# Kernel tuning notes

Measured on AMD Instinct MI355X. Metric: run time of the kernel, lower is better.

The kernel has to match this reference:

```python
import jax, jax.numpy as jnp
import numpy as np

B, S, D = 4, 1024, 1024
NH, HD = 16, 64            # heads, head_dim
R = 4                      # channel_shrink_ratio
LD, LHD = D // R, HD // R  # layout hidden, layout head_dim
MAXP = 2048                # max_position_embeddings


def _heads(x, nh, hd):
    # [B,S,nh*hd] -> [B,nh,S,hd]
    b, s, _ = x.shape
    return x.reshape(b, s, nh, hd).transpose(0, 2, 1, 3)


def setup_inputs() -> dict:
    key = jax.random.key(0)
    ks = jax.random.split(key, 17)
    init = lambda k, shape: jax.random.normal(k, shape, dtype=jnp.float32) * 0.02
    return {
        "hidden_states": init(ks[0], (B, S, D)),
        "layout_inputs": init(ks[1], (B, S, LD)),
        "attention_mask": jnp.zeros((B, 1, 1, S), jnp.float32),
        # text-stream projections (parameterized as x @ W + b, W:[in,out])
        "wq": init(ks[2], (D, D)), "bq": jnp.zeros((D,), jnp.float32),
        "wk": init(ks[3], (D, D)), "bk": jnp.zeros((D,), jnp.float32),
        "wv": init(ks[4], (D, D)), "bv": jnp.zeros((D,), jnp.float32),
        # layout-stream projections
        "lwq": init(ks[5], (LD, LD)), "lbq": jnp.zeros((LD,), jnp.float32),
        "lwk": init(ks[6], (LD, LD)), "lbk": jnp.zeros((LD,), jnp.float32),
        "lwv": init(ks[7], (LD, LD)), "lbv": jnp.zeros((LD,), jnp.float32),
        # relative distance embedding table [2*MAXP-1, HD]
        "dist_emb": init(ks[8], (2 * MAXP - 1, HD)),
    }


def reference(hidden_states, layout_inputs, attention_mask,
              wq, bq, wk, bk, wv, bv,
              lwq, lbq, lwk, lbk, lwv, lbv, dist_emb):
    # projections + head split
    q = _heads(hidden_states @ wq + bq, NH, HD)   # [B,NH,S,HD]
    k = _heads(hidden_states @ wk + bk, NH, HD)
    v = _heads(hidden_states @ wv + bv, NH, HD)
    lq = _heads(layout_inputs @ lwq + lbq, NH, LHD)  # [B,NH,S,LHD]
    lk = _heads(layout_inputs @ lwk + lbk, NH, LHD)
    lv = _heads(layout_inputs @ lwv + lbv, NH, LHD)

    # raw QK^T scores for both streams
    scores = jnp.einsum('bhld,bhrd->bhlr', q, k)        # [B,NH,S,S]
    lscores = jnp.einsum('bhld,bhrd->bhlr', lq, lk)     # [B,NH,S,S]

    # relative_key positional bias on text stream
    idx = jnp.arange(S)[:, None] - jnp.arange(S)[None, :] + (MAXP - 1)  # [S,S]
    pe = dist_emb[idx]                                   # [S,S,HD]
    scores = scores + jnp.einsum('bhld,lrd->bhlr', q, pe)

    # cross-stream score fusion: both streams share the same combined scores
    combined = scores / np.sqrt(HD) + lscores / np.sqrt(LHD) + attention_mask
    probs = jax.nn.softmax(combined, axis=-1)            # dropout_p = 0 (eval)

    ctx = jnp.einsum('bhlr,bhrd->bhld', probs, v)        # [B,NH,S,HD]
    ctx = ctx.transpose(0, 2, 1, 3).reshape(B, S, D)
    lctx = jnp.einsum('bhlr,bhrd->bhld', probs, lv)      # [B,NH,S,LHD]
    lctx = lctx.transpose(0, 2, 1, 3).reshape(B, S, LD)
    return (ctx, lctx)
```

## Files before the change

kernel.cpp:

```cpp
#include <hip/hip_runtime.h>
#include <math.h>

#define S_LEN 1024
#define NHEAD 16
#define HDIM 64
#define LHDIM 16

typedef __bf16 bf16;
typedef bf16 bf16x4 __attribute__((ext_vector_type(4)));
typedef bf16 bf16x8 __attribute__((ext_vector_type(8)));
typedef float f32x4 __attribute__((ext_vector_type(4)));

#define MFMA16(a, b, c) __builtin_amdgcn_mfma_f32_16x16x32_bf16(a, b, c, 0, 0, 0)

__device__ __forceinline__ void gl2lds16(const void* g, void* l)
{
    __builtin_amdgcn_global_load_lds(
        (const __attribute__((address_space(1))) unsigned int*)g,
        (__attribute__((address_space(3))) unsigned int*)l,
        16, 0, 0);
}

__global__ __launch_bounds__(256)
void prep_kernel(const float* __restrict__ hs,   bf16* __restrict__ hsb,
                 const float* __restrict__ lin,  bf16* __restrict__ linb,
                 const float* __restrict__ de32, bf16* __restrict__ de,
                 const float* __restrict__ W0, const float* __restrict__ W1,
                 const float* __restrict__ W2,
                 bf16* __restrict__ T0, bf16* __restrict__ T1, bf16* __restrict__ T2,
                 const float* __restrict__ LW0, const float* __restrict__ LW1,
                 const float* __restrict__ LW2,
                 bf16* __restrict__ LT0, bf16* __restrict__ LT1, bf16* __restrict__ LT2)
{
    const int bx = blockIdx.x;
    const int t  = threadIdx.x;

    if (bx < 5376) {
        const float* in; bf16* out; int i; int n4;
        if (bx < 4096)      { in = hs;   out = hsb;  i = bx * 256 + t;          n4 = 1048576; }
        else if (bx < 5120) { in = lin;  out = linb; i = (bx - 4096) * 256 + t; n4 = 262144; }
        else                { in = de32; out = de;   i = (bx - 5120) * 256 + t; n4 = 65520; }
        if (i < n4) {
            float4 v = *(const float4*)&in[(size_t)i * 4];
            bf16x4 o = { (bf16)v.x, (bf16)v.y, (bf16)v.z, (bf16)v.w };
            *(bf16x4*)&out[(size_t)i * 4] = o;
        }
        return;
    }

    const int bt = bx - 5376;
    const float* W; bf16* T; int K, N, k0, n0;
    if (bt < 768) {
        int proj = bt >> 8, tile = bt & 255;
        W = proj == 0 ? W0 : (proj == 1 ? W1 : W2);
        T = proj == 0 ? T0 : (proj == 1 ? T1 : T2);
        K = N = 1024; k0 = (tile >> 4) << 6; n0 = (tile & 15) << 6;
    } else {
        int b2 = bt - 768;
        int proj = b2 >> 4, tile = b2 & 15;
        W = proj == 0 ? LW0 : (proj == 1 ? LW1 : LW2);
        T = proj == 0 ? LT0 : (proj == 1 ? LT1 : LT2);
        K = N = 256; k0 = (tile >> 2) << 6; n0 = (tile & 3) << 6;
    }

    __shared__ float Ts[64][65];
    #pragma unroll
    for (int p = 0; p < 4; p++) {
        int li = p * 256 + t;
        int r  = li >> 4, c4 = (li & 15) << 2;
        float4 v = *(const float4*)&W[(size_t)(k0 + r) * N + n0 + c4];
        Ts[r][c4 + 0] = v.x; Ts[r][c4 + 1] = v.y;
        Ts[r][c4 + 2] = v.z; Ts[r][c4 + 3] = v.w;
    }
    __syncthreads();

    int r2 = t >> 2, ks = (t & 3) << 4;
    bf16x8 o0, o1;
    #pragma unroll
    for (int u = 0; u < 8; u++) o0[u] = (bf16)Ts[ks + u][r2];
    #pragma unroll
    for (int u = 0; u < 8; u++) o1[u] = (bf16)Ts[ks + 8 + u][r2];
    *(bf16x8*)&T[(size_t)(n0 + r2) * K + k0 + ks]     = o0;
    *(bf16x8*)&T[(size_t)(n0 + r2) * K + k0 + ks + 8] = o1;
}

__global__ __launch_bounds__(256, 3)
void projm_all_kernel(const bf16* __restrict__ Xt, const bf16* __restrict__ Xl,
                      const bf16* __restrict__ Wt0, const float* __restrict__ B0,
                      const bf16* __restrict__ Wt1, const float* __restrict__ B1,
                      const bf16* __restrict__ Wt2, const float* __restrict__ B2,
                      const bf16* __restrict__ LWt0, const float* __restrict__ LB0,
                      const bf16* __restrict__ LWt1, const float* __restrict__ LB1,
                      const bf16* __restrict__ LWt2, const float* __restrict__ LB2,
                      bf16* __restrict__ O0, bf16* __restrict__ O1, bf16* __restrict__ O2,
                      bf16* __restrict__ LO0, bf16* __restrict__ LO1, bf16* __restrict__ LO2)
{
    const int z = blockIdx.z;
    const bf16* X; const bf16* Wt; const float* Bi; bf16* O;
    float scale; int KDIM, nshift, n0;
    const int m0 = blockIdx.y << 7;

    if (z < 3) {
        X = Xt; KDIM = 1024; nshift = 6;
        Wt = z == 0 ? Wt0 : (z == 1 ? Wt1 : Wt2);
        Bi = z == 0 ? B0  : (z == 1 ? B1  : B2);
        O  = z == 0 ? O0  : (z == 1 ? O1  : O2);
        scale = z == 0 ? 0.125f : 1.0f;
        n0 = blockIdx.x << 7;
    } else {
        if (blockIdx.x >= 6) return;
        int proj = blockIdx.x >> 1;
        X = Xl; KDIM = 256; nshift = 4;
        Wt = proj == 0 ? LWt0 : (proj == 1 ? LWt1 : LWt2);
        Bi = proj == 0 ? LB0  : (proj == 1 ? LB1  : LB2);
        O  = proj == 0 ? LO0  : (proj == 1 ? LO1  : LO2);
        scale = proj == 0 ? 0.25f : 1.0f;
        n0 = (blockIdx.x & 1) << 7;
    }
    const int nhdm = (1 << nshift) - 1;

    __shared__ bf16 As[128 * 32];
    __shared__ bf16 Bs[128 * 32];

    const int t    = threadIdx.x;
    const int wv   = t >> 6;
    const int l64  = t & 63;
    const int ln   = l64 & 15;
    const int quad = l64 >> 4;
    const int wm   = wv & 1;
    const int wn   = wv >> 1;

    const int arow = l64 >> 2;
    const int koff = (l64 & 3) << 3;

    f32x4 acc[4][4];
    #pragma unroll
    for (int i = 0; i < 4; i++)
        #pragma unroll
        for (int j = 0; j < 4; j++) acc[i][j] = (f32x4)0.0f;

    for (int k0 = 0; k0 < KDIM; k0 += 32) {
        #pragma unroll
        for (int c = 0; c < 2; c++) {
            int g = (c * 4 + wv) << 4;
            gl2lds16(&X [(size_t)(m0 + g + arow) * KDIM + k0 + koff], &As[(c * 4 + wv) * 512]);
            gl2lds16(&Wt[(size_t)(n0 + g + arow) * KDIM + k0 + koff], &Bs[(c * 4 + wv) * 512]);
        }
        __syncthreads();

        bf16x8 af[4], bfv[4];
        #pragma unroll
        for (int mt = 0; mt < 4; mt++)
            af[mt] = *(const bf16x8*)&As[(wm * 64 + mt * 16 + ln) * 32 + quad * 8];
        #pragma unroll
        for (int nt = 0; nt < 4; nt++)
            bfv[nt] = *(const bf16x8*)&Bs[(wn * 64 + nt * 16 + ln) * 32 + quad * 8];
        #pragma unroll
        for (int mt = 0; mt < 4; mt++)
            #pragma unroll
            for (int nt = 0; nt < 4; nt++)
                acc[mt][nt] = MFMA16(af[mt], bfv[nt], acc[mt][nt]);
        __syncthreads();
    }

    #pragma unroll
    for (int nt = 0; nt < 4; nt++) {
        int n  = n0 + wn * 64 + nt * 16 + ln;
        float bia = Bi[n];
        int hh = n >> nshift;
        int dd = n & nhdm;
        #pragma unroll
        for (int mt = 0; mt < 4; mt++) {
            #pragma unroll
            for (int reg = 0; reg < 4; reg++) {
                int m  = m0 + wm * 64 + mt * 16 + quad * 4 + reg;
                int bb = m >> 10;
                int s  = m & 1023;
                O[((size_t)((bb * NHEAD + hh) << 10) + s) * (nhdm + 1) + dd] =
                    (bf16)((acc[mt][nt][reg] + bia) * scale);
            }
        }
    }
}

__global__ __launch_bounds__(512, 2)
void attn_kernel(const bf16* __restrict__ qg, const bf16* __restrict__ kg,
                 const bf16* __restrict__ vg, const bf16* __restrict__ lqg,
                 const bf16* __restrict__ lkg, const bf16* __restrict__ lvg,
                 const float* __restrict__ maskg, const bf16* __restrict__ demb,
                 float* __restrict__ octx, float* __restrict__ olctx)
{
    __shared__ bf16 Ks[2][64][104];
    __shared__ bf16 VsT[2][64][72];
    __shared__ bf16 LVsT[2][16][72];
    __shared__ bf16 Ps[256][72];

    const int t    = threadIdx.x;
    const int w    = t >> 6;
    const int lane = t & 63;
    const int ln   = lane & 15;
    const int quad = lane >> 4;
    const int mb0  = w << 5;

    const int lid = blockIdx.x;
    const int bh  = (lid & 7) * 8 + (lid >> 5);
    const int xt  = (lid >> 3) & 3;
    const int b   = bh >> 4;
    const int h   = bh & 15;
    const int l0  = xt << 8;

    const bf16* qb  = qg  + (size_t)bh * (S_LEN * HDIM);
    const bf16* kb  = kg  + (size_t)bh * (S_LEN * HDIM);
    const bf16* vb  = vg  + (size_t)bh * (S_LEN * HDIM);
    const bf16* lqb = lqg + (size_t)bh * (S_LEN * LHDIM);
    const bf16* lkb = lkg + (size_t)bh * (S_LEN * LHDIM);
    const bf16* lvb = lvg + (size_t)bh * (S_LEN * LHDIM);

    bf16x8 zer, one8;
    #pragma unroll
    for (int u = 0; u < 8; u++) { zer[u] = (bf16)0.0f; one8[u] = (bf16)1.0f; }

    if (t < 128) {
        int row = t >> 1, h8 = (t & 1) << 3;
        *(bf16x8*)&Ks[0][row][80 + h8] = zer;
        *(bf16x8*)&Ks[1][row][80 + h8] = zer;
    }

    bf16x8 af[2][3];
    #pragma unroll
    for (int st = 0; st < 2; st++) {
        const int qrow = l0 + mb0 + st * 16 + ln;
        af[st][0] = *(const bf16x8*)&qb[(size_t)qrow * HDIM + quad * 8];
        af[st][1] = *(const bf16x8*)&qb[(size_t)qrow * HDIM + 32 + quad * 8];
        af[st][2] = (quad < 2) ? *(const bf16x8*)&lqb[(size_t)qrow * LHDIM + quad * 8] : zer;
    }

    const int krow = t >> 3, kc8 = (t & 7) << 3;
    const int lkrow = t >> 1, lh8 = (t & 1) << 3;
    const int vr = t & 63,  vd8 = w << 3;
    const int lvr = t & 63, lvd8 = (w & 1) << 3;

    f32x4 co[2][4];
    f32x4 cl[2];
    f32x4 la[2];
    #pragma unroll
    for (int st = 0; st < 2; st++) {
        #pragma unroll
        for (int i = 0; i < 4; i++) co[st][i] = (f32x4)0.0f;
        cl[st] = (f32x4)0.0f;
        la[st] = (f32x4)0.0f;
    }

    for (int r0 = 0; r0 < S_LEN; r0 += 128) {
        bf16x8 kx[2], lkx[2], vx[2], lvx[2];
        float msv[2][4];
        #pragma unroll
        for (int sub = 0; sub < 2; sub++) {
            const int rr = r0 + sub * 64;
            kx[sub]  = *(const bf16x8*)&kb[(size_t)(rr + krow) * HDIM + kc8];
            lkx[sub] = (t < 128) ? *(const bf16x8*)&lkb[(size_t)(rr + lkrow) * LHDIM + lh8] : zer;
            vx[sub]  = *(const bf16x8*)&vb[(size_t)(rr + vr) * HDIM + vd8];
            lvx[sub] = (t < 128) ? *(const bf16x8*)&lvb[(size_t)(rr + lvr) * LHDIM + lvd8] : zer;
            #pragma unroll
            for (int nt = 0; nt < 4; nt++)
                msv[sub][nt] = maskg[b * S_LEN + rr + nt * 16 + ln];
        }

        __syncthreads();

        #pragma unroll
        for (int sub = 0; sub < 2; sub++) {
            *(bf16x8*)&Ks[sub][krow][kc8] = kx[sub];
            if (t < 128) *(bf16x8*)&Ks[sub][lkrow][64 + lh8] = lkx[sub];
            #pragma unroll
            for (int u = 0; u < 8; u++) VsT[sub][vd8 + u][vr] = vx[sub][u];
            if (t < 128) {
                #pragma unroll
                for (int u = 0; u < 8; u++) LVsT[sub][lvd8 + u][lvr] = lvx[sub][u];
            }
        }

        __syncthreads();

        #pragma unroll
        for (int sub = 0; sub < 2; sub++) {
            const int jb = l0 - (r0 + sub * 64) + 1984;

            bf16x8 ef[6][2];
            #pragma unroll
            for (int ct2 = 0; ct2 < 6; ct2++) {
                const bf16* ep = &demb[(size_t)(jb + mb0 + ct2 * 16 + ln) * HDIM + quad * 8];
                ef[ct2][0] = *(const bf16x8*)ep;
                ef[ct2][1] = *(const bf16x8*)(ep + 32);
            }

            bf16x8 kf[4][3];
            #pragma unroll
            for (int nt = 0; nt < 4; nt++) {
                const bf16* kr = &Ks[sub][nt * 16 + ln][quad * 8];
                kf[nt][0] = *(const bf16x8*)(kr);
                kf[nt][1] = *(const bf16x8*)(kr + 32);
                kf[nt][2] = *(const bf16x8*)(kr + 64);
            }

            #pragma unroll
            for (int st = 0; st < 2; st++) {
                const int mq = mb0 + st * 16;

                f32x4 hh[5];
                #pragma unroll
                for (int ct = 0; ct < 5; ct++) {
                    hh[ct] = (f32x4)0.0f;
                    hh[ct] = MFMA16(af[st][0], ef[st + ct][0], hh[ct]);
                    hh[ct] = MFMA16(af[st][1], ef[st + ct][1], hh[ct]);
                }

                f32x4 sc[4];
                #pragma unroll
                for (int nt = 0; nt < 4; nt++) {
                    sc[nt] = (f32x4)0.0f;
                    sc[nt] = MFMA16(af[st][0], kf[nt][0], sc[nt]);
                    sc[nt] = MFMA16(af[st][1], kf[nt][1], sc[nt]);
                    sc[nt] = MFMA16(af[st][2], kf[nt][2], sc[nt]);
                }

                float bias[4][4];
                #pragma unroll
                for (int reg = 0; reg < 4; reg++) {
                    int d = quad * 4 + reg - ln + 63;
                    int srcLane = (quad << 4) | (d & 15);
                    float sh[5];
                    #pragma unroll
                    for (int ct = 0; ct < 5; ct++)
                        sh[ct] = __shfl(hh[ct][reg], srcLane);
                    bool f4 = (d >> 4) == 4;
                    #pragma unroll
                    for (int nt = 0; nt < 4; nt++)
                        bias[nt][reg] = f4 ? sh[4 - nt] : sh[3 - nt];
                }

                #pragma unroll
                for (int nt = 0; nt < 4; nt++)
                    #pragma unroll
                    for (int reg = 0; reg < 4; reg++) {
                        float p = __expf(sc[nt][reg] + bias[nt][reg] + msv[sub][nt]);
                        Ps[mq + quad * 4 + reg][nt * 16 + ln] = (bf16)p;
                    }
            }

            bf16x8 vf[4][2], lvf[2];
            #pragma unroll
            for (int ks = 0; ks < 2; ks++) {
                #pragma unroll
                for (int nt = 0; nt < 4; nt++)
                    vf[nt][ks] = *(const bf16x8*)&VsT[sub][nt * 16 + ln][ks * 32 + quad * 8];
                lvf[ks] = *(const bf16x8*)&LVsT[sub][ln][ks * 32 + quad * 8];
            }

            #pragma unroll
            for (int st = 0; st < 2; st++) {
                const int mq = mb0 + st * 16;
                #pragma unroll
                for (int ks = 0; ks < 2; ks++) {
                    bf16x8 ap = *(const bf16x8*)&Ps[mq + ln][ks * 32 + quad * 8];
                    cl[st] = MFMA16(ap, lvf[ks], cl[st]);
                    la[st] = MFMA16(ap, one8, la[st]);
                    #pragma unroll
                    for (int nt = 0; nt < 4; nt++)
                        co[st][nt] = MFMA16(ap, vf[nt][ks], co[st][nt]);
                }
            }
        }
    }

    #pragma unroll
    for (int st = 0; st < 2; st++)
        #pragma unroll
        for (int reg = 0; reg < 4; reg++) {
            int s = l0 + mb0 + st * 16 + quad * 4 + reg;
            float inv = 1.0f / la[st][reg];
            #pragma unroll
            for (int nt = 0; nt < 4; nt++)
                octx[(size_t)(b * S_LEN + s) * 1024 + h * 64 + nt * 16 + ln] = co[st][nt][reg] * inv;
            olctx[(size_t)(b * S_LEN + s) * 256 + h * 16 + ln] = cl[st][reg] * inv;
        }
}

extern "C" void kernel_launch(void* const* d_in, const int* in_sizes, int n_in,
                              void* d_out, int out_size, void* d_ws, size_t ws_size,
                              hipStream_t stream)
{
    (void)in_sizes; (void)n_in; (void)out_size; (void)ws_size;

    const float* hs   = (const float*)d_in[0];
    const float* lin  = (const float*)d_in[1];
    const float* mask = (const float*)d_in[2];
    const float* wq  = (const float*)d_in[3];  const float* bq  = (const float*)d_in[4];
    const float* wk  = (const float*)d_in[5];  const float* bk  = (const float*)d_in[6];
    const float* wv  = (const float*)d_in[7];  const float* bv  = (const float*)d_in[8];
    const float* lwq = (const float*)d_in[9];  const float* lbq = (const float*)d_in[10];
    const float* lwk = (const float*)d_in[11]; const float* lbk = (const float*)d_in[12];
    const float* lwv = (const float*)d_in[13]; const float* lbv = (const float*)d_in[14];
    const float* demb = (const float*)d_in[15];

    bf16* ws = (bf16*)d_ws;
    bf16* q    = ws;
    bf16* k    = ws + 4194304;
    bf16* v    = ws + 8388608;
    bf16* lq   = ws + 12582912;
    bf16* lk   = ws + 13631488;
    bf16* lv   = ws + 14680064;
    bf16* de   = ws + 15728640;
    bf16* hsb  = ws + 16000000;
    bf16* linb = ws + 20194304;
    bf16* wqt  = ws + 21242880;
    bf16* wkt  = ws + 22291456;
    bf16* wvt  = ws + 23340032;
    bf16* lwqt = ws + 24388608;
    bf16* lwkt = ws + 24454144;
    bf16* lwvt = ws + 24519680;

    prep_kernel<<<dim3(6192), 256, 0, stream>>>(
        hs, hsb, lin, linb, demb, de,
        wq, wk, wv, wqt, wkt, wvt, lwq, lwk, lwv, lwqt, lwkt, lwvt);

    projm_all_kernel<<<dim3(8, 32, 4), 256, 0, stream>>>(
        hsb, linb,
        wqt, bq, wkt, bk, wvt, bv,
        lwqt, lbq, lwkt, lbk, lwvt, lbv,
        q, k, v, lq, lk, lv);

    float* octx  = (float*)d_out;
    float* olctx = (float*)d_out + 4194304;
    attn_kernel<<<dim3(256), 512, 0, stream>>>(
        q, k, v, lq, lk, lv, mask, de, octx, olctx);
}
```

Baseline: 210.8 us.

## Prefetch next K/V tile into registers and remap projection blocks across XCDs

The attention loop now issues global loads for the next 128-row K/V/layout/mask tile right after the current tile is staged into LDS, so the load latency overlaps the current tile's MFMA and softmax work. Mask values are copied to a separate register set so the prefetch does not overwrite values still in use. Separately, the projection GEMM now remaps a flattened block id so that blocks dispatched to the same XCD cover adjacent M rows, which is meant to improve L2 reuse. The prefetch raises register pressure, which may lower occupancy.

Result: slower. 241.5 us (+14.6%).

```diff
diff --git a/kernel.cpp b/kernel.cpp
--- a/kernel.cpp
+++ b/kernel.cpp
@@ -95,10 +95,17 @@
                       bf16* __restrict__ O0, bf16* __restrict__ O1, bf16* __restrict__ O2,
                       bf16* __restrict__ LO0, bf16* __restrict__ LO1, bf16* __restrict__ LO2)
 {
-    const int z = blockIdx.z;
+    const int f   = blockIdx.x + (blockIdx.y << 3) + (blockIdx.z << 8);
+    const int xcd = f & 7;
+    const int rr_ = f >> 3;
+    const int by  = (xcd << 2) | (rr_ & 3);
+    const int bxx = (rr_ >> 2) & 7;
+    const int bz  = rr_ >> 5;
+
+    const int z = bz;
     const bf16* X; const bf16* Wt; const float* Bi; bf16* O;
     float scale; int KDIM, nshift, n0;
-    const int m0 = blockIdx.y << 7;
+    const int m0 = by << 7;
 
     if (z < 3) {
         X = Xt; KDIM = 1024; nshift = 6;
@@ -106,16 +113,16 @@
         Bi = z == 0 ? B0  : (z == 1 ? B1  : B2);
         O  = z == 0 ? O0  : (z == 1 ? O1  : O2);
         scale = z == 0 ? 0.125f : 1.0f;
-        n0 = blockIdx.x << 7;
+        n0 = bxx << 7;
     } else {
-        if (blockIdx.x >= 6) return;
-        int proj = blockIdx.x >> 1;
+        if (bxx >= 6) return;
+        int proj = bxx >> 1;
         X = Xl; KDIM = 256; nshift = 4;
         Wt = proj == 0 ? LWt0 : (proj == 1 ? LWt1 : LWt2);
         Bi = proj == 0 ? LB0  : (proj == 1 ? LB1  : LB2);
         O  = proj == 0 ? LO0  : (proj == 1 ? LO1  : LO2);
         scale = proj == 0 ? 0.25f : 1.0f;
-        n0 = (blockIdx.x & 1) << 7;
+        n0 = (bxx & 1) << 7;
     }
     const int nhdm = (1 << nshift) - 1;
 
@@ -251,21 +258,28 @@
         la[st] = (f32x4)0.0f;
     }
 
+    bf16x8 kx[2], lkx[2], vx[2], lvx[2];
+    float msv[2][4];
+    float msc[2][4];
+
+#define LOAD_TILE_REGS(R0BASE)                                                          \
+    do {                                                                                \
+        _Pragma("unroll")                                                               \
+        for (int sub_ = 0; sub_ < 2; sub_++) {                                          \
+            const int rr = (R0BASE) + sub_ * 64;                                        \
+            kx[sub_]  = *(const bf16x8*)&kb[(size_t)(rr + krow) * HDIM + kc8];          \
+            lkx[sub_] = (t < 128) ? *(const bf16x8*)&lkb[(size_t)(rr + lkrow) * LHDIM + lh8] : zer; \
+            vx[sub_]  = *(const bf16x8*)&vb[(size_t)(rr + vr) * HDIM + vd8];            \
+            lvx[sub_] = (t < 128) ? *(const bf16x8*)&lvb[(size_t)(rr + lvr) * LHDIM + lvd8] : zer;  \
+            _Pragma("unroll")                                                           \
+            for (int nt_ = 0; nt_ < 4; nt_++)                                           \
+                msv[sub_][nt_] = maskg[b * S_LEN + rr + nt_ * 16 + ln];                 \
+        }                                                                               \
+    } while (0)
+
+    LOAD_TILE_REGS(0);
+
     for (int r0 = 0; r0 < S_LEN; r0 += 128) {
-        bf16x8 kx[2], lkx[2], vx[2], lvx[2];
-        float msv[2][4];
-        #pragma unroll
-        for (int sub = 0; sub < 2; sub++) {
-            const int rr = r0 + sub * 64;
-            kx[sub]  = *(const bf16x8*)&kb[(size_t)(rr + krow) * HDIM + kc8];
-            lkx[sub] = (t < 128) ? *(const bf16x8*)&lkb[(size_t)(rr + lkrow) * LHDIM + lh8] : zer;
-            vx[sub]  = *(const bf16x8*)&vb[(size_t)(rr + vr) * HDIM + vd8];
-            lvx[sub] = (t < 128) ? *(const bf16x8*)&lvb[(size_t)(rr + lvr) * LHDIM + lvd8] : zer;
-            #pragma unroll
-            for (int nt = 0; nt < 4; nt++)
-                msv[sub][nt] = maskg[b * S_LEN + rr + nt * 16 + ln];
-        }
-
         __syncthreads();
 
         #pragma unroll
@@ -281,6 +295,12 @@
         }
 
         __syncthreads();
+
+        #pragma unroll
+        for (int sub = 0; sub < 2; sub++)
+            #pragma unroll
+            for (int nt = 0; nt < 4; nt++) msc[sub][nt] = msv[sub][nt];
+        if (r0 + 128 < S_LEN) LOAD_TILE_REGS(r0 + 128);
 
         #pragma unroll
         for (int sub = 0; sub < 2; sub++) {
@@ -343,7 +363,7 @@
                 for (int nt = 0; nt < 4; nt++)
                     #pragma unroll
                     for (int reg = 0; reg < 4; reg++) {
-                        float p = __expf(sc[nt][reg] + bias[nt][reg] + msv[sub][nt]);
+                        float p = __expf(sc[nt][reg] + bias[nt][reg] + msc[sub][nt]);
                         Ps[mq + quad * 4 + reg][nt * 16 + ln] = (bf16)p;
                     }
             }
@@ -372,6 +392,7 @@
             }
         }
     }
+#undef LOAD_TILE_REGS
 
     #pragma unroll
     for (int st = 0; st < 2; st++)
```
